# Kernel optimization log

Measured on AMD Instinct MI355X. Metric: run time of the kernel, lower is better.

## Reference

```python
import jax, jax.numpy as jnp
import numpy as np

B, N, DIN, DOUT, EIN, EOUT = 8, 256, 64, 64, 64, 64


def setup_inputs() -> dict:
    key = jax.random.key(0)
    ks = jax.random.split(key, 9)
    A = jax.random.randint(ks[0], (B, N, N), 0, 2).astype(jnp.float32)  # {0,1} connectivity
    emb_node = jax.random.normal(ks[1], (B, N, DIN), dtype=jnp.float32)
    emb_edge = jax.random.normal(ks[2], (B, N, N, EIN), dtype=jnp.float32)
    s_n = 1.0 / np.sqrt(DIN)
    s_e = 1.0 / np.sqrt(EIN)
    Wn = jax.random.uniform(ks[3], (DIN, DOUT), minval=-s_n, maxval=s_n)
    bn = jax.random.uniform(ks[4], (DOUT,), minval=-s_n, maxval=s_n)
    Wsn = jax.random.uniform(ks[5], (DIN, DOUT), minval=-s_n, maxval=s_n)
    bsn = jax.random.uniform(ks[6], (DOUT,), minval=-s_n, maxval=s_n)
    We = jax.random.uniform(ks[7], (EIN, EOUT), minval=-s_e, maxval=s_e)
    be = jax.random.uniform(ks[8], (EOUT,), minval=-s_e, maxval=s_e)
    return {"A": A, "emb_node": emb_node, "emb_edge": emb_edge,
            "Wn": Wn, "bn": bn, "Wsn": Wsn, "bsn": bsn, "We": We, "be": be}


def reference(A, emb_node, emb_edge, Wn, bn, Wsn, bsn, We, be):
    # mode=1 (default) of ChannelIndependentConv
    node_x = emb_node @ Wn + bn          # [B,N,DOUT]
    node_sx = emb_node @ Wsn + bsn       # [B,N,DOUT]
    edge_x = emb_edge @ We + be          # [B,N,N,EOUT]
    # mask edges by connectivity, then channel-independent aggregation:
    # out[b,i,c] = sum_j A[b,i,j] * edge_x[b,i,j,c] * node_x[b,j,c]
    Ae = A[..., None] * edge_x           # [B,N,N,EOUT]
    agg = jnp.einsum('bijc,bjc->bic', Ae, node_x)  # [B,N,DOUT]
    node_out = jax.nn.relu(agg) + jax.nn.relu(node_sx)
    edge_out = jax.nn.relu(edge_x)
    return node_out, edge_out
```

## Files before the change

kernel.cpp:

```cpp
#include <hip/hip_runtime.h>

#define BN   2048
#define NN   256
#define CH   64
#define NCHK 8

typedef __attribute__((ext_vector_type(8))) short short8;
typedef __attribute__((ext_vector_type(4))) float fv4;

static __device__ inline short f2bf(float f) {
  unsigned u = __float_as_uint(f);
  u += 0x7FFF + ((u >> 16) & 1);
  return (short)(u >> 16);
}

static __device__ inline short8 cvt_frag(fv4 a, fv4 b) {
  union { short8 s; unsigned u[4]; } r;
  asm("v_cvt_pk_bf16_f32 %0, %1, %2" : "=v"(r.u[0]) : "v"(a[0]), "v"(a[1]));
  asm("v_cvt_pk_bf16_f32 %0, %1, %2" : "=v"(r.u[1]) : "v"(a[2]), "v"(a[3]));
  asm("v_cvt_pk_bf16_f32 %0, %1, %2" : "=v"(r.u[2]) : "v"(b[0]), "v"(b[1]));
  asm("v_cvt_pk_bf16_f32 %0, %1, %2" : "=v"(r.u[3]) : "v"(b[2]), "v"(b[3]));
  return r.s;
}

#define GLOAD16(gp, lp)                                                        \
  __builtin_amdgcn_global_load_lds(                                            \
      (const __attribute__((address_space(1))) unsigned*)(gp),                 \
      (__attribute__((address_space(3))) unsigned*)(lp), 16, 0, 0)

#define WAITV(N) asm volatile("s_waitcnt vmcnt(" #N ")" ::: "memory")

__global__ __launch_bounds__(256) void node_kernel(
    const float* __restrict__ emb_node, const float* __restrict__ Wn,
    const float* __restrict__ bn, const float* __restrict__ Wsn,
    const float* __restrict__ bsn, float* __restrict__ node_x,
    float* __restrict__ rsx) {
  __shared__ float s_emb[4][CH];
  __shared__ float s_Wn[CH * CH];
  __shared__ float s_Ws[CH * CH];
  const int tid = threadIdx.x;
  const int r = tid >> 6;
  const int c = tid & 63;
  const int row = blockIdx.x * 4 + r;
#pragma unroll
  for (int i = 0; i < 4; ++i) {
    *(fv4*)&s_Wn[(i * 256 + tid) * 4] = *(const fv4*)&Wn[(i * 256 + tid) * 4];
    *(fv4*)&s_Ws[(i * 256 + tid) * 4] = *(const fv4*)&Wsn[(i * 256 + tid) * 4];
  }
  s_emb[r][c] = emb_node[row * CH + c];
  __syncthreads();
  float a1 = bn[c], a2 = bsn[c];
#pragma unroll
  for (int k = 0; k < CH; ++k) {
    const float e = s_emb[r][k];
    a1 = fmaf(e, s_Wn[k * CH + c], a1);
    a2 = fmaf(e, s_Ws[k * CH + c], a2);
  }
  node_x[row * CH + c] = a1;
  rsx[row * CH + c] = fmaxf(a2, 0.0f);
}

__global__ __launch_bounds__(256, 4) void edge_mfma_kernel(
    const float* __restrict__ A, const float* __restrict__ emb_edge,
    const float* __restrict__ We, const float* __restrict__ be,
    const float* __restrict__ node_x, const float* __restrict__ rsx,
    float* __restrict__ node_out, float* __restrict__ edge_out) {
  const int bi   = blockIdx.x;
  const int b    = bi >> 8;
  const int tid  = threadIdx.x;
  const int lane = tid & 63;
  const int wave = tid >> 6;
  const int l15  = lane & 15;
  const int quad = lane >> 4;
  const int c    = wave * 16 + l15;

  __shared__ __align__(16) float s_e[3][2048];
  __shared__ __align__(16) float s_n[3][2048];
  __shared__ __align__(16) float s_Af[NN];

  const float* __restrict__ ee = emb_edge + (size_t)bi * NN * CH;
  float*       __restrict__ eo = edge_out + (size_t)bi * NN * CH;
  const float* __restrict__ nx = node_x + (size_t)b * NN * CH;

  const float aval = A[(size_t)bi * NN + tid];
  s_Af[tid] = aval;

  short8 bfrag[2];
#pragma unroll
  for (int h = 0; h < 2; ++h)
#pragma unroll
    for (int j = 0; j < 8; ++j)
      bfrag[h][j] = f2bf(We[(h * 32 + quad * 8 + j) * CH + c]);
  const float bias = be[c];

  const int rowA = wave * 8 + (lane >> 4);
  const int rowB = rowA + 4;
  const int ibq  = (lane & 15) * 16;
  const int offA = rowA * 256 + (ibq ^ ((rowA & 15) << 4));
  const int offB = rowB * 256 + (ibq ^ ((rowB & 15) << 4));
  const int swz = l15 << 4;
  const int o0 = (quad * 32) ^ swz;
  const int o1 = (quad * 32 + 16) ^ swz;
  const int o2 = (128 + quad * 32) ^ swz;
  const int o3 = (144 + quad * 32) ^ swz;
  int nxo[4];
#pragma unroll
  for (int r = 0; r < 4; ++r)
    nxo[r] = (quad * 4 + r) * 256 + ((c * 4) ^ ((quad * 4 + r) << 4));

#define STAGE(T, D)                                                            \
  {                                                                            \
    const char* eb_ = (const char*)ee + (T) * 8192;                            \
    const char* nb_ = (const char*)nx + (T) * 8192;                            \
    GLOAD16(eb_ + offA, (char*)&s_e[(D)][0] + wave * 2048);                    \
    GLOAD16(eb_ + offB, (char*)&s_e[(D)][0] + wave * 2048 + 1024);             \
    GLOAD16(nb_ + offA, (char*)&s_n[(D)][0] + wave * 2048);                    \
    GLOAD16(nb_ + offB, (char*)&s_n[(D)][0] + wave * 2048 + 1024);             \
  }

  STAGE(0, 0)
  STAGE(1, 1)

  float agg = 0.0f;

#define COMPUTE(CHK, D)                                                        \
  {                                                                            \
    _Pragma("unroll") for (int h = 0; h < 2; ++h) {                            \
      const char* eb_ = (const char*)&s_e[(D)][0] + (h * 16 + l15) * 256;      \
      const fv4 a0 = *(const fv4*)(eb_ + o0);                                  \
      const fv4 a1 = *(const fv4*)(eb_ + o1);                                  \
      const fv4 a2 = *(const fv4*)(eb_ + o2);                                  \
      const fv4 a3 = *(const fv4*)(eb_ + o3);                                  \
      const short8 af0 = cvt_frag(a0, a1);                                     \
      const short8 af1 = cvt_frag(a2, a3);                                     \
      fv4 acc = {bias, bias, bias, bias};                                      \
      acc = __builtin_amdgcn_mfma_f32_16x16x32_bf16(af0, bfrag[0], acc, 0,0,0);\
      acc = __builtin_amdgcn_mfma_f32_16x16x32_bf16(af1, bfrag[1], acc, 0,0,0);\
      const int j0 = (CHK) * 32 + h * 16;                                      \
      const fv4 av = *(const fv4*)&s_Af[j0 + quad * 4];                        \
      const char* nb_ = (const char*)&s_n[(D)][0] + h * 4096;                  \
      _Pragma("unroll") for (int r = 0; r < 4; ++r) {                          \
        const float nxv = *(const float*)(nb_ + nxo[r]);                       \
        const int row = j0 + quad * 4 + r;                                     \
        const float ex = acc[r];                          \
        eo[row * CH + c] = fmaxf(ex, 0.0f);                                    \
        agg = fmaf(av[r] * ex, nxv, agg);                                      \
      }                                                                        \
    }                                                                          \
  }

#define ITER(CHK, NW, PF)                                                      \
  {                                                                            \
    WAITV(NW);                                                                 \
    __builtin_amdgcn_s_barrier();                                              \
    if (PF) STAGE((CHK) + 2, ((CHK) + 2) % 3)                                  \
    asm volatile("" ::: "memory");                 \
    COMPUTE(CHK, (CHK) % 3)                                                    \
  }

  asm volatile("s_waitcnt vmcnt(4) lgkmcnt(0)" ::: "memory");
  __builtin_amdgcn_s_barrier();
  STAGE(2, 2)
  asm volatile("" ::: "memory");
  COMPUTE(0, 0)

  ITER(1, 12, 1)
  ITER(2, 20, 1)
  ITER(3, 20, 1)
  ITER(4, 20, 1)
  ITER(5, 20, 1)
  ITER(6, 20, 0)
  ITER(7, 16, 0)

#undef ITER
#undef COMPUTE
#undef STAGE

  agg += __shfl_xor(agg, 16, 64);
  agg += __shfl_xor(agg, 32, 64);
  if (quad == 0) {
    node_out[(size_t)bi * CH + c] =
        fmaxf(agg, 0.0f) + rsx[(size_t)bi * CH + c];
  }
}

extern "C" void kernel_launch(void* const* d_in, const int* in_sizes, int n_in,
                              void* d_out, int out_size, void* d_ws, size_t ws_size,
                              hipStream_t stream) {
  const float* A        = (const float*)d_in[0];
  const float* emb_node = (const float*)d_in[1];
  const float* emb_edge = (const float*)d_in[2];
  const float* Wn       = (const float*)d_in[3];
  const float* bn       = (const float*)d_in[4];
  const float* Wsn      = (const float*)d_in[5];
  const float* bsn      = (const float*)d_in[6];
  const float* We       = (const float*)d_in[7];
  const float* be       = (const float*)d_in[8];

  float* node_out = (float*)d_out;
  float* edge_out = (float*)d_out + (size_t)BN * CH;

  float* node_x = (float*)d_ws;
  float* rsx    = (float*)d_ws + (size_t)BN * CH;

  hipLaunchKernelGGL(node_kernel, dim3(BN / 4), dim3(256), 0, stream,
                     emb_node, Wn, bn, Wsn, bsn, node_x, rsx);
  hipLaunchKernelGGL(edge_mfma_kernel, dim3(BN), dim3(256), 0, stream,
                     A, emb_edge, We, be, node_x, rsx, node_out, edge_out);
}
```

Before: 258.2 us.

## Swap MFMA operands so each lane owns 4 channels, enabling vectorized edge stores

Transposes the MFMA formulation (weights as A operand, edges as B), so each lane's accumulator holds 4 consecutive output channels for one edge row instead of 4 rows for one channel. This turns the scalar edge_out stores into 16-byte vector stores and the node_x LDS reads into a single fv4 load. The vmcnt wait counts are reduced to match the smaller number of outstanding stores per iteration. The cost is a longer cross-lane reduction at the end, 4 values over 4 shuffle steps.

```diff
diff --git a/kernel.cpp b/kernel.cpp
--- a/kernel.cpp
+++ b/kernel.cpp
@@ -3,7 +3,6 @@
 #define BN   2048
 #define NN   256
 #define CH   64
-#define NCHK 8
 
 typedef __attribute__((ext_vector_type(8))) short short8;
 typedef __attribute__((ext_vector_type(4))) float fv4;
@@ -72,7 +71,7 @@
   const int wave = tid >> 6;
   const int l15  = lane & 15;
   const int quad = lane >> 4;
-  const int c    = wave * 16 + l15;
+  const int cq   = wave * 16 + quad * 4;
 
   __shared__ __align__(16) float s_e[3][2048];
   __shared__ __align__(16) float s_n[3][2048];
@@ -85,13 +84,13 @@
   const float aval = A[(size_t)bi * NN + tid];
   s_Af[tid] = aval;
 
-  short8 bfrag[2];
+  short8 wfrag[2];
 #pragma unroll
   for (int h = 0; h < 2; ++h)
 #pragma unroll
     for (int j = 0; j < 8; ++j)
-      bfrag[h][j] = f2bf(We[(h * 32 + quad * 8 + j) * CH + c]);
-  const float bias = be[c];
+      wfrag[h][j] = f2bf(We[(h * 32 + quad * 8 + j) * CH + wave * 16 + l15]);
+  const fv4 biasv = *(const fv4*)&be[cq];
 
   const int rowA = wave * 8 + (lane >> 4);
   const int rowB = rowA + 4;
@@ -103,10 +102,7 @@
   const int o1 = (quad * 32 + 16) ^ swz;
   const int o2 = (128 + quad * 32) ^ swz;
   const int o3 = (144 + quad * 32) ^ swz;
-  int nxo[4];
-#pragma unroll
-  for (int r = 0; r < 4; ++r)
-    nxo[r] = (quad * 4 + r) * 256 + ((c * 4) ^ ((quad * 4 + r) << 4));
+  const int nxo = (cq * 4) ^ swz;
 
 #define STAGE(T, D)                                                            \
   {                                                                            \
@@ -121,7 +117,7 @@
   STAGE(0, 0)
   STAGE(1, 1)
 
-  float agg = 0.0f;
+  fv4 agg = {0.f, 0.f, 0.f, 0.f};
 
 #define COMPUTE(CHK, D)                                                        \
   {                                                                            \
@@ -133,19 +129,20 @@
       const fv4 a3 = *(const fv4*)(eb_ + o3);                                  \
       const short8 af0 = cvt_frag(a0, a1);                                     \
       const short8 af1 = cvt_frag(a2, a3);                                     \
-      fv4 acc = {bias, bias, bias, bias};                                      \
-      acc = __builtin_amdgcn_mfma_f32_16x16x32_bf16(af0, bfrag[0], acc, 0,0,0);\
-      acc = __builtin_amdgcn_mfma_f32_16x16x32_bf16(af1, bfrag[1], acc, 0,0,0);\
-      const int j0 = (CHK) * 32 + h * 16;                                      \
-      const fv4 av = *(const fv4*)&s_Af[j0 + quad * 4];                        \
-      const char* nb_ = (const char*)&s_n[(D)][0] + h * 4096;                  \
+      fv4 acc = biasv;                                       \
+      acc = __builtin_amdgcn_mfma_f32_16x16x32_bf16(wfrag[0], af0, acc, 0,0,0);\
+      acc = __builtin_amdgcn_mfma_f32_16x16x32_bf16(wfrag[1], af1, acc, 0,0,0);\
+      const int j = (CHK) * 32 + h * 16 + l15;            \
+      const float av = s_Af[j];                          \
+      const fv4 nxv =                                                          \
+          *(const fv4*)((const char*)&s_n[(D)][0] + h * 4096 +                 \
+                        l15 * 256 + nxo);                                      \
+      fv4 rl;                                                                  \
       _Pragma("unroll") for (int r = 0; r < 4; ++r) {                          \
-        const float nxv = *(const float*)(nb_ + nxo[r]);                       \
-        const int row = j0 + quad * 4 + r;                                     \
-        const float ex = acc[r];                          \
-        eo[row * CH + c] = fmaxf(ex, 0.0f);                                    \
-        agg = fmaf(av[r] * ex, nxv, agg);                                      \
+        rl[r] = fmaxf(acc[r], 0.0f);                                           \
+        agg[r] = fmaf(av * acc[r], nxv[r], agg[r]);                            \
       }                                                                        \
+      *(fv4*)(eo + j * CH + cq) = rl;        \
     }                                                                          \
   }
 
@@ -164,23 +161,31 @@
   asm volatile("" ::: "memory");
   COMPUTE(0, 0)
 
-  ITER(1, 12, 1)
-  ITER(2, 20, 1)
-  ITER(3, 20, 1)
-  ITER(4, 20, 1)
-  ITER(5, 20, 1)
-  ITER(6, 20, 0)
-  ITER(7, 16, 0)
+  ITER(1, 6, 1)
+  ITER(2, 8, 1)
+  ITER(3, 8, 1)
+  ITER(4, 8, 1)
+  ITER(5, 8, 1)
+  ITER(6, 8, 0)
+  ITER(7, 4, 0)
 
 #undef ITER
 #undef COMPUTE
 #undef STAGE
 
-  agg += __shfl_xor(agg, 16, 64);
-  agg += __shfl_xor(agg, 32, 64);
-  if (quad == 0) {
-    node_out[(size_t)bi * CH + c] =
-        fmaxf(agg, 0.0f) + rsx[(size_t)bi * CH + c];
+#pragma unroll
+  for (int r = 0; r < 4; ++r) {
+    agg[r] += __shfl_xor(agg[r], 1, 64);
+    agg[r] += __shfl_xor(agg[r], 2, 64);
+    agg[r] += __shfl_xor(agg[r], 4, 64);
+    agg[r] += __shfl_xor(agg[r], 8, 64);
+  }
+  if (l15 == 0) {
+    const fv4 rs = *(const fv4*)&rsx[(size_t)bi * CH + cq];
+    fv4 out;
+#pragma unroll
+    for (int r = 0; r < 4; ++r) out[r] = fmaxf(agg[r], 0.0f) + rs[r];
+    *(fv4*)&node_out[(size_t)bi * CH + cq] = out;
   }
 }
 
```

New measurement: 261.1 us. About the same (+1.2%).
